# Optimization experiments

Measured on AMD Instinct MI355X. Metric: run time of the kernel, lower is better.

## Reference

```python
import jax, jax.numpy as jnp
import numpy as np

N, DEG, D_FEAT, D_OUT = 50000, 32, 128, 256

def setup_inputs() -> dict:
    key = jax.random.key(0)
    k1, k2, k3 = jax.random.split(key, 3)
    features = jax.random.normal(k1, (N, D_FEAT), dtype=jnp.float32)
    edge_look_up = jax.random.randint(k2, (N, DEG), 0, N, dtype=jnp.int64)
    # glorot-uniform kernel, shape (2*D_FEAT, D_OUT)
    limit = np.sqrt(6.0 / (2 * D_FEAT + D_OUT)).astype(np.float32)
    kernel = jax.random.uniform(k3, (2 * D_FEAT, D_OUT), dtype=jnp.float32,
                                minval=-limit, maxval=limit)
    return {"features": features, "edge_look_up": edge_look_up, "kernel": kernel}

def reference(features, edge_look_up, kernel):
    # [1] neighborhood aggregation: gather neighbor features and mean-reduce
    neigh = features[edge_look_up]          # [N, DEG, D_FEAT] (irregular gather)
    agg = jnp.mean(neigh, axis=1)           # [N, D_FEAT]
    # [2] concat self features with aggregated neighbor vectors
    out = jnp.concatenate([features, agg], axis=-1)  # [N, 2*D_FEAT]
    # [4] dense matmul + [5] relu activation
    return jax.nn.relu(out @ kernel)        # [N, D_OUT]
```

## Files before the change

kernel.cpp:

```cpp
#include <hip/hip_runtime.h>

#define NN  50000
#define DEG 32
#define DF  128
#define DO  256
#define FEAT4 (NN * DF / 4)

typedef __bf16 bf16x8 __attribute__((ext_vector_type(8)));
typedef float  f32x4  __attribute__((ext_vector_type(4)));
typedef float  f32x2  __attribute__((ext_vector_type(2)));
typedef unsigned short u16x8 __attribute__((ext_vector_type(8)));

#if defined(__has_builtin)
#if __has_builtin(__builtin_amdgcn_cvt_pk_f32_fp8) && __has_builtin(__builtin_amdgcn_cvt_pk_fp8_f32)
#define HW_FP8 1
#endif
#endif
#ifndef HW_FP8
#define HW_FP8 0
#endif

__device__ __forceinline__ unsigned short f2bf(float f) {
    unsigned u = __float_as_uint(f);
    u += 0x7FFF + ((u >> 16) & 1);
    return (unsigned short)(u >> 16);
}

#if !HW_FP8
__device__ __forceinline__ unsigned enc1_fp8(float f) {
    unsigned u = __float_as_uint(f);
    unsigned s = (u >> 31) << 7;
    float a = fabsf(f);
    if (!(a > 0.f)) return s;
    if (a >= 448.f) return s | 0x7E;
    u = __float_as_uint(a);
    int e = (int)((u >> 23) & 255) - 127;
    if (e < -6) {
        unsigned m = (unsigned)(a * 512.f + 0.5f);
        if (m >= 8) return s | 0x08;
        return s | m;
    }
    unsigned mant = (u >> 20) & 7;
    unsigned rnd  = ((u >> 19) & 1) & (((u & 0x7FFFF) != 0) | ((u >> 20) & 1));
    unsigned enc  = ((unsigned)(e + 7) << 3) | mant;
    return s | (enc + rnd);
}
__device__ __forceinline__ float dec1_fp8(unsigned b) {
    unsigned s = (b >> 7) & 1, e = (b >> 3) & 15, m = b & 7;
    float v = (e == 0) ? (float)m * 0.001953125f
                       : __uint_as_float(((e - 7 + 127) << 23) | (m << 20));
    return s ? -v : v;
}
#endif

__device__ __forceinline__ unsigned enc4_fp8(float4 v) {
#if HW_FP8
    int pk = 0;
    pk = __builtin_amdgcn_cvt_pk_fp8_f32(v.x, v.y, pk, false);
    pk = __builtin_amdgcn_cvt_pk_fp8_f32(v.z, v.w, pk, true);
    return (unsigned)pk;
#else
    return enc1_fp8(v.x) | (enc1_fp8(v.y) << 8) | (enc1_fp8(v.z) << 16) | (enc1_fp8(v.w) << 24);
#endif
}

__global__ __launch_bounds__(256) void convert_kernel(
    const float* __restrict__ feat, const float* __restrict__ W,
    unsigned* __restrict__ feat8, unsigned short* __restrict__ featb,
    unsigned short* __restrict__ Wt)
{
    const int gid = blockIdx.x * 256 + threadIdx.x;
    if (gid < FEAT4) {
        const float4 v = ((const float4*)feat)[gid];
        feat8[gid] = enc4_fp8(v);
        ushort4 o;
        o.x = f2bf(v.x); o.y = f2bf(v.y); o.z = f2bf(v.z); o.w = f2bf(v.w);
        ((ushort4*)featb)[gid] = o;
    } else {
        const int t = gid - FEAT4;
        if (t < DO * DO) {
            const int n = t >> 8, k = t & 255;
            Wt[n * DO + k] = f2bf(W[k * DO + n]);
        }
    }
}

__global__ __launch_bounds__(256) void agg_kernel(
    const unsigned* __restrict__ feat8,
    const int*      __restrict__ edges,
    unsigned short* __restrict__ aggb)
{
    const int node = blockIdx.x * 16 + (threadIdx.x >> 4);
    const int l    = threadIdx.x & 15;
    const int* e   = edges + node * DEG;

    float a[8] = {0.f, 0.f, 0.f, 0.f, 0.f, 0.f, 0.f, 0.f};
    #pragma unroll
    for (int d = 0; d < DEG; ++d) {
        const int idx = e[d];
        const uint2 pk = *(const uint2*)(feat8 + (size_t)idx * (DF / 4) + l * 2);
#if HW_FP8
        const f32x2 v0 = __builtin_amdgcn_cvt_pk_f32_fp8((int)pk.x, false);
        const f32x2 v1 = __builtin_amdgcn_cvt_pk_f32_fp8((int)pk.x, true);
        const f32x2 v2 = __builtin_amdgcn_cvt_pk_f32_fp8((int)pk.y, false);
        const f32x2 v3 = __builtin_amdgcn_cvt_pk_f32_fp8((int)pk.y, true);
        a[0] += v0[0]; a[1] += v0[1]; a[2] += v1[0]; a[3] += v1[1];
        a[4] += v2[0]; a[5] += v2[1]; a[6] += v3[0]; a[7] += v3[1];
#else
        #pragma unroll
        for (int j = 0; j < 4; ++j) a[j]     += dec1_fp8((pk.x >> (8 * j)) & 255);
        #pragma unroll
        for (int j = 0; j < 4; ++j) a[4 + j] += dec1_fp8((pk.y >> (8 * j)) & 255);
#endif
    }

    const float s = 1.0f / (float)DEG;
    u16x8 o;
    #pragma unroll
    for (int j = 0; j < 8; ++j) o[j] = f2bf(a[j] * s);
    *(u16x8*)(aggb + (size_t)node * DF + l * 8) = o;
}

#define BM  128
#define BN  128
#define LDA 72

__global__ __launch_bounds__(256) void gemm_kernel(
    const unsigned short* __restrict__ featb,
    const unsigned short* __restrict__ aggb,
    const unsigned short* __restrict__ Wt,
    float*                __restrict__ out)
{
    __shared__ __align__(16) unsigned short Asw[BM * LDA];
    __shared__ __align__(16) unsigned short Bsw[BN * LDA];

    const int tid  = threadIdx.x;
    const int m0   = blockIdx.x * BM;
    const int c0   = blockIdx.y * BN;
    const int wave = tid >> 6, lane = tid & 63;
    const int quad = lane >> 4, lr = lane & 15;
    const int wm   = (wave & 1) * 64;
    const int wn   = (wave >> 1) * 64;

    const int srow = tid >> 3;
    const int sseg = (tid & 7) * 8;

    f32x4 acc[4][4] = {};

    for (int kc = 0; kc < 4; ++kc) {
        const unsigned short* srcA = (kc < 2) ? (featb + kc * 64)
                                              : (aggb + (kc - 2) * 64);
        const unsigned short* srcB = Wt + kc * 64;

        __syncthreads();
        #pragma unroll
        for (int p = 0; p < 4; ++p) {
            const int r = p * 32 + srow;
            int node = m0 + r;
            if (node >= NN) node = NN - 1;
            const float4 va = *(const float4*)(srcA + (size_t)node * DF + sseg);
            *(float4*)(Asw + r * LDA + sseg) = va;
            const float4 vb = *(const float4*)(srcB + (size_t)(c0 + r) * DO + sseg);
            *(float4*)(Bsw + r * LDA + sseg) = vb;
        }
        __syncthreads();

        #pragma unroll
        for (int kk = 0; kk < 64; kk += 32) {
            bf16x8 af[4], bfr[4];
            #pragma unroll
            for (int i = 0; i < 4; ++i) {
                af[i]  = *(const bf16x8*)(Asw + (wm + i * 16 + lr) * LDA + kk + quad * 8);
                bfr[i] = *(const bf16x8*)(Bsw + (wn + i * 16 + lr) * LDA + kk + quad * 8);
            }
            #pragma unroll
            for (int mi = 0; mi < 4; ++mi)
                #pragma unroll
                for (int ni = 0; ni < 4; ++ni)
                    acc[mi][ni] = __builtin_amdgcn_mfma_f32_16x16x32_bf16(
                        af[mi], bfr[ni], acc[mi][ni], 0, 0, 0);
        }
    }

    #pragma unroll
    for (int mi = 0; mi < 4; ++mi) {
        #pragma unroll
        for (int r = 0; r < 4; ++r) {
            const int row = m0 + wm + mi * 16 + quad * 4 + r;
            if (row < NN) {
                #pragma unroll
                for (int ni = 0; ni < 4; ++ni) {
                    out[(size_t)row * DO + c0 + wn + ni * 16 + lr] =
                        fmaxf(acc[mi][ni][r], 0.f);
                }
            }
        }
    }
}

extern "C" void kernel_launch(void* const* d_in, const int* in_sizes, int n_in,
                              void* d_out, int out_size, void* d_ws, size_t ws_size,
                              hipStream_t stream)
{
    const float* feat  = (const float*)d_in[0];
    const int*   edges = (const int*)d_in[1];
    const float* W     = (const float*)d_in[2];
    float*       out   = (float*)d_out;

    unsigned short* aggb  = (unsigned short*)d_ws;
    unsigned*       feat8 = (unsigned*)(aggb + (size_t)NN * DF);
    unsigned short* featb = (unsigned short*)(feat8 + (size_t)NN * DF / 4);
    unsigned short* Wt    = featb + (size_t)NN * DF;

    convert_kernel<<<(FEAT4 + DO * DO + 255) / 256, 256, 0, stream>>>(
        feat, W, feat8, featb, Wt);
    agg_kernel<<<NN / 16, 256, 0, stream>>>(feat8, edges, aggb);

    dim3 grid((NN + BM - 1) / BM, DO / BN);
    gemm_kernel<<<grid, 256, 0, stream>>>(featb, aggb, Wt, out);
}
```

Before: 124.3 us.

## Fuse neighbor aggregation into GEMM kernel and convert self features on the fly

Merges the aggregation and GEMM kernels into one kernel. Each 512-thread block gathers and averages neighbors for 64 nodes into registers, then writes them into shared memory as the A tile for the second half of K. Self features are converted from fp32 to bf16 while being loaded, which removes the bf16 feature copy and the aggb round trip through global memory. The block now covers all 256 output columns (BM=64, BN=256), so W is reloaded per block and the gather latency is no longer overlapped with other blocks' GEMM work.

```diff
diff --git a/kernel.cpp b/kernel.cpp
--- a/kernel.cpp
+++ b/kernel.cpp
@@ -66,16 +66,12 @@
 
 __global__ __launch_bounds__(256) void convert_kernel(
     const float* __restrict__ feat, const float* __restrict__ W,
-    unsigned* __restrict__ feat8, unsigned short* __restrict__ featb,
-    unsigned short* __restrict__ Wt)
+    unsigned* __restrict__ feat8, unsigned short* __restrict__ Wt)
 {
     const int gid = blockIdx.x * 256 + threadIdx.x;
     if (gid < FEAT4) {
         const float4 v = ((const float4*)feat)[gid];
         feat8[gid] = enc4_fp8(v);
-        ushort4 o;
-        o.x = f2bf(v.x); o.y = f2bf(v.y); o.z = f2bf(v.z); o.w = f2bf(v.w);
-        ((ushort4*)featb)[gid] = o;
     } else {
         const int t = gid - FEAT4;
         if (t < DO * DO) {
@@ -85,96 +81,109 @@
     }
 }
 
-__global__ __launch_bounds__(256) void agg_kernel(
-    const unsigned* __restrict__ feat8,
-    const int*      __restrict__ edges,
-    unsigned short* __restrict__ aggb)
-{
-    const int node = blockIdx.x * 16 + (threadIdx.x >> 4);
-    const int l    = threadIdx.x & 15;
-    const int* e   = edges + node * DEG;
-
-    float a[8] = {0.f, 0.f, 0.f, 0.f, 0.f, 0.f, 0.f, 0.f};
-    #pragma unroll
-    for (int d = 0; d < DEG; ++d) {
-        const int idx = e[d];
-        const uint2 pk = *(const uint2*)(feat8 + (size_t)idx * (DF / 4) + l * 2);
-#if HW_FP8
-        const f32x2 v0 = __builtin_amdgcn_cvt_pk_f32_fp8((int)pk.x, false);
-        const f32x2 v1 = __builtin_amdgcn_cvt_pk_f32_fp8((int)pk.x, true);
-        const f32x2 v2 = __builtin_amdgcn_cvt_pk_f32_fp8((int)pk.y, false);
-        const f32x2 v3 = __builtin_amdgcn_cvt_pk_f32_fp8((int)pk.y, true);
-        a[0] += v0[0]; a[1] += v0[1]; a[2] += v1[0]; a[3] += v1[1];
-        a[4] += v2[0]; a[5] += v2[1]; a[6] += v3[0]; a[7] += v3[1];
-#else
-        #pragma unroll
-        for (int j = 0; j < 4; ++j) a[j]     += dec1_fp8((pk.x >> (8 * j)) & 255);
-        #pragma unroll
-        for (int j = 0; j < 4; ++j) a[4 + j] += dec1_fp8((pk.y >> (8 * j)) & 255);
-#endif
-    }
-
-    const float s = 1.0f / (float)DEG;
-    u16x8 o;
-    #pragma unroll
-    for (int j = 0; j < 8; ++j) o[j] = f2bf(a[j] * s);
-    *(u16x8*)(aggb + (size_t)node * DF + l * 8) = o;
-}
-
-#define BM  128
-#define BN  128
-#define LDA 72
-
-__global__ __launch_bounds__(256) void gemm_kernel(
-    const unsigned short* __restrict__ featb,
-    const unsigned short* __restrict__ aggb,
+#define BM  64
+#define BN  256
+#define LDT 72
+
+__global__ __launch_bounds__(512) void fused_kernel(
+    const float*          __restrict__ feat,
+    const unsigned*       __restrict__ feat8,
+    const int*            __restrict__ edges,
     const unsigned short* __restrict__ Wt,
     float*                __restrict__ out)
 {
-    __shared__ __align__(16) unsigned short Asw[BM * LDA];
-    __shared__ __align__(16) unsigned short Bsw[BN * LDA];
-
-    const int tid  = threadIdx.x;
-    const int m0   = blockIdx.x * BM;
-    const int c0   = blockIdx.y * BN;
+    __shared__ __align__(16) unsigned short Asw[BM * LDT];
+    __shared__ __align__(16) unsigned short Bsw[BN * LDT];
+
+    const int tid = threadIdx.x;
+    const int m0  = blockIdx.x * BM;
+
+    const int l = tid & 15;
+    u16x8 aggr[2];
+    #pragma unroll
+    for (int pass = 0; pass < 2; ++pass) {
+        int node = m0 + pass * 32 + (tid >> 4);
+        if (node >= NN) node = NN - 1;
+        const int* e = edges + node * DEG;
+        float a[8] = {0.f, 0.f, 0.f, 0.f, 0.f, 0.f, 0.f, 0.f};
+        #pragma unroll
+        for (int d = 0; d < DEG; ++d) {
+            const int idx = e[d];
+            const uint2 pk = *(const uint2*)(feat8 + (size_t)idx * (DF / 4) + l * 2);
+#if HW_FP8
+            const f32x2 v0 = __builtin_amdgcn_cvt_pk_f32_fp8((int)pk.x, false);
+            const f32x2 v1 = __builtin_amdgcn_cvt_pk_f32_fp8((int)pk.x, true);
+            const f32x2 v2 = __builtin_amdgcn_cvt_pk_f32_fp8((int)pk.y, false);
+            const f32x2 v3 = __builtin_amdgcn_cvt_pk_f32_fp8((int)pk.y, true);
+            a[0] += v0[0]; a[1] += v0[1]; a[2] += v1[0]; a[3] += v1[1];
+            a[4] += v2[0]; a[5] += v2[1]; a[6] += v3[0]; a[7] += v3[1];
+#else
+            #pragma unroll
+            for (int j = 0; j < 4; ++j) a[j]     += dec1_fp8((pk.x >> (8 * j)) & 255);
+            #pragma unroll
+            for (int j = 0; j < 4; ++j) a[4 + j] += dec1_fp8((pk.y >> (8 * j)) & 255);
+#endif
+        }
+        const float s = 1.0f / (float)DEG;
+        #pragma unroll
+        for (int j = 0; j < 8; ++j) aggr[pass][j] = f2bf(a[j] * s);
+    }
+
     const int wave = tid >> 6, lane = tid & 63;
     const int quad = lane >> 4, lr = lane & 15;
-    const int wm   = (wave & 1) * 64;
+    const int wm   = (wave & 1) * 32;
     const int wn   = (wave >> 1) * 64;
 
-    const int srow = tid >> 3;
-    const int sseg = (tid & 7) * 8;
-
-    f32x4 acc[4][4] = {};
+    f32x4 acc[2][4] = {};
 
     for (int kc = 0; kc < 4; ++kc) {
-        const unsigned short* srcA = (kc < 2) ? (featb + kc * 64)
-                                              : (aggb + (kc - 2) * 64);
-        const unsigned short* srcB = Wt + kc * 64;
-
         __syncthreads();
-        #pragma unroll
-        for (int p = 0; p < 4; ++p) {
-            const int r = p * 32 + srow;
+
+        if (kc < 2) {
+            const int r = tid >> 3;
+            const int c = (tid & 7) * 8;
             int node = m0 + r;
             if (node >= NN) node = NN - 1;
-            const float4 va = *(const float4*)(srcA + (size_t)node * DF + sseg);
-            *(float4*)(Asw + r * LDA + sseg) = va;
-            const float4 vb = *(const float4*)(srcB + (size_t)(c0 + r) * DO + sseg);
-            *(float4*)(Bsw + r * LDA + sseg) = vb;
-        }
+            const float* src = feat + (size_t)node * DF + kc * 64 + c;
+            const float4 v0 = *(const float4*)(src);
+            const float4 v1 = *(const float4*)(src + 4);
+            u16x8 o;
+            o[0] = f2bf(v0.x); o[1] = f2bf(v0.y); o[2] = f2bf(v0.z); o[3] = f2bf(v0.w);
+            o[4] = f2bf(v1.x); o[5] = f2bf(v1.y); o[6] = f2bf(v1.z); o[7] = f2bf(v1.w);
+            *(u16x8*)(Asw + r * LDT + c) = o;
+        } else {
+            if ((l >> 3) == (kc - 2)) {
+                const int c = (l & 7) * 8;
+                #pragma unroll
+                for (int pass = 0; pass < 2; ++pass) {
+                    const int r = pass * 32 + (tid >> 4);
+                    *(u16x8*)(Asw + r * LDT + c) = aggr[pass];
+                }
+            }
+        }
+
+        #pragma unroll
+        for (int it = 0; it < 4; ++it) {
+            const int sidx = it * 512 + tid;
+            const int r = sidx >> 3;
+            const int c = (sidx & 7) * 8;
+            *(u16x8*)(Bsw + r * LDT + c) =
+                *(const u16x8*)(Wt + (size_t)r * DO + kc * 64 + c);
+        }
+
         __syncthreads();
 
         #pragma unroll
         for (int kk = 0; kk < 64; kk += 32) {
-            bf16x8 af[4], bfr[4];
-            #pragma unroll
-            for (int i = 0; i < 4; ++i) {
-                af[i]  = *(const bf16x8*)(Asw + (wm + i * 16 + lr) * LDA + kk + quad * 8);
-                bfr[i] = *(const bf16x8*)(Bsw + (wn + i * 16 + lr) * LDA + kk + quad * 8);
-            }
-            #pragma unroll
-            for (int mi = 0; mi < 4; ++mi)
+            bf16x8 af[2], bfr[4];
+            #pragma unroll
+            for (int i = 0; i < 2; ++i)
+                af[i] = *(const bf16x8*)(Asw + (wm + i * 16 + lr) * LDT + kk + quad * 8);
+            #pragma unroll
+            for (int i = 0; i < 4; ++i)
+                bfr[i] = *(const bf16x8*)(Bsw + (wn + i * 16 + lr) * LDT + kk + quad * 8);
+            #pragma unroll
+            for (int mi = 0; mi < 2; ++mi)
                 #pragma unroll
                 for (int ni = 0; ni < 4; ++ni)
                     acc[mi][ni] = __builtin_amdgcn_mfma_f32_16x16x32_bf16(
@@ -183,14 +192,14 @@
     }
 
     #pragma unroll
-    for (int mi = 0; mi < 4; ++mi) {
+    for (int mi = 0; mi < 2; ++mi) {
         #pragma unroll
         for (int r = 0; r < 4; ++r) {
             const int row = m0 + wm + mi * 16 + quad * 4 + r;
             if (row < NN) {
                 #pragma unroll
                 for (int ni = 0; ni < 4; ++ni) {
-                    out[(size_t)row * DO + c0 + wn + ni * 16 + lr] =
+                    out[(size_t)row * DO + wn + ni * 16 + lr] =
                         fmaxf(acc[mi][ni][r], 0.f);
                 }
             }
@@ -207,15 +216,12 @@
     const float* W     = (const float*)d_in[2];
     float*       out   = (float*)d_out;
 
-    unsigned short* aggb  = (unsigned short*)d_ws;
-    unsigned*       feat8 = (unsigned*)(aggb + (size_t)NN * DF);
-    unsigned short* featb = (unsigned short*)(feat8 + (size_t)NN * DF / 4);
-    unsigned short* Wt    = featb + (size_t)NN * DF;
+    unsigned*       feat8 = (unsigned*)d_ws;
+    unsigned short* Wt    = (unsigned short*)(feat8 + (size_t)NN * DF / 4);
 
     convert_kernel<<<(FEAT4 + DO * DO + 255) / 256, 256, 0, stream>>>(
-        feat, W, feat8, featb, Wt);
-    agg_kernel<<<NN / 16, 256, 0, stream>>>(feat8, edges, aggb);
-
-    dim3 grid((NN + BM - 1) / BM, DO / BN);
-    gemm_kernel<<<grid, 256, 0, stream>>>(featb, aggb, Wt, out);
-}
+        feat, W, feat8, Wt);
+
+    fused_kernel<<<(NN + BM - 1) / BM, 512, 0, stream>>>(
+        feat, feat8, edges, Wt, out);
+}
```

New measurement: 128.5 us. 1.03x slower.
